# Kernel optimization log

Hardware: AMD Instinct MI355X
Metric: run time of the kernel (lower is better)

Reference implementation:

```python
import jax, jax.numpy as jnp
import numpy as np

N_EMBD = 768
HEAD_SIZE = 64

def setup_inputs() -> dict:
    key = jax.random.key(0)
    ks = jax.random.split(key, 9)
    B, S = 8, 2048
    scale = 1.0 / np.sqrt(N_EMBD)
    return {
        "q": jax.random.normal(ks[0], (B, S, N_EMBD), jnp.float32),
        "k": jax.random.normal(ks[1], (B, S, N_EMBD), jnp.float32),
        "v": jax.random.normal(ks[2], (B, S, N_EMBD), jnp.float32),
        "Wq": jax.random.normal(ks[3], (N_EMBD, HEAD_SIZE), jnp.float32) * scale,
        "bq": jnp.zeros((HEAD_SIZE,), jnp.float32),
        "Wk": jax.random.normal(ks[4], (N_EMBD, HEAD_SIZE), jnp.float32) * scale,
        "bk": jnp.zeros((HEAD_SIZE,), jnp.float32),
        "Wv": jax.random.normal(ks[5], (N_EMBD, HEAD_SIZE), jnp.float32) * scale,
        "bv": jnp.zeros((HEAD_SIZE,), jnp.float32),
    }

def reference(q, k, v, Wq, bq, Wk, bk, Wv, bv):
    # NOTE: original scales by sqrt(C) where C = n_embd (input dim), not head_size.
    C = q.shape[-1]
    qi = q @ Wq + bq  # [B,S,H]
    ki = k @ Wk + bk
    vi = v @ Wv + bv
    att = jnp.einsum('bsh,bth->bst', qi, ki) / jnp.sqrt(jnp.float32(C))
    att = jax.nn.softmax(att, axis=-1)
    out = jnp.einsum('bst,bth->bsh', att, vi)
    return out
```

## Files before the change

kernel.cpp:

```cpp
#include <hip/hip_runtime.h>

#define Bn 8
#define Sn 2048
#define Cn 768
#define Hn 64

typedef __attribute__((ext_vector_type(8))) short bf16x8;
typedef __attribute__((ext_vector_type(4))) float f32x4;

__device__ __forceinline__ unsigned short f2bf(float x) {
  unsigned int u = __builtin_bit_cast(unsigned int, x);
  u += 0x7FFFu + ((u >> 16) & 1u);
  return (unsigned short)(u >> 16);
}

__global__ __launch_bounds__(256) void wconv(const float* __restrict__ Wq,
                                             const float* __restrict__ Wk,
                                             const float* __restrict__ Wv,
                                             unsigned short* __restrict__ Wt) {
  int idx = blockIdx.x * 256 + threadIdx.x;
  int mat = idx / (Cn * Hn);
  int rem = idx - mat * (Cn * Hn);
  int c = rem / Hn, h = rem - c * Hn;
  const float* W = (mat == 0) ? Wq : (mat == 1) ? Wk : Wv;
  Wt[mat * (Hn * Cn) + h * Cn + c] = f2bf(W[rem]);
}

__global__ __launch_bounds__(256) void proj(const float* __restrict__ q,
                                            const float* __restrict__ k,
                                            const float* __restrict__ v,
                                            const float* __restrict__ bq,
                                            const float* __restrict__ bk,
                                            const float* __restrict__ bv,
                                            const unsigned short* __restrict__ Wt,
                                            unsigned short* __restrict__ qi,
                                            unsigned short* __restrict__ ki,
                                            unsigned short* __restrict__ vi) {
  const int mat  = blockIdx.x >> 8;
  const int row0 = (blockIdx.x & 255) * 64;
  const float* X    = (mat == 0) ? q  : (mat == 1) ? k  : v;
  const float* bias = (mat == 0) ? bq : (mat == 1) ? bk : bv;
  unsigned short* Y = (mat == 0) ? qi : (mat == 1) ? ki : vi;
  const unsigned short* Wm = Wt + mat * (Hn * Cn);
  const float scale = (mat == 0) ? 0.03608439182435161f : 1.0f;

  __shared__ __align__(16) unsigned char Xs[64 * 128];
  __shared__ __align__(16) unsigned char Ws[64 * 128];

  const int tid  = threadIdx.x;
  const int lane = tid & 63;
  const int w    = tid >> 6;
  const int col  = lane & 15;
  const int grp  = lane >> 4;

  f32x4 acc[4] = {};

  for (int kc = 0; kc < 12; ++kc) {
    __syncthreads();
#pragma unroll
    for (int i = 0; i < 4; ++i) {
      int f4 = tid + i * 256;
      int r  = f4 >> 4;
      int c4 = f4 & 15;
      float4 xv = *(const float4*)(X + (size_t)(row0 + r) * Cn + kc * 64 + c4 * 4);
      ushort4 hv;
      hv.x = f2bf(xv.x); hv.y = f2bf(xv.y); hv.z = f2bf(xv.z); hv.w = f2bf(xv.w);
      *(ushort4*)(Xs + r * 128 + ((c4 * 8) ^ ((r & 7) << 4))) = hv;
    }
    {
      int r = tid >> 2;
      int p = tid & 3;
      const uint4* src = (const uint4*)(Wm + (size_t)r * Cn + kc * 64);
      uint4 a  = src[p * 2];
      uint4 b2 = src[p * 2 + 1];
      *(uint4*)(Ws + r * 128 + ((p * 32) ^ ((r & 7) << 4)))        = a;
      *(uint4*)(Ws + r * 128 + (((p * 32) + 16) ^ ((r & 7) << 4))) = b2;
    }
    __syncthreads();
    const int rloc = w * 16 + col;
#pragma unroll
    for (int ks = 0; ks < 2; ++ks) {
      bf16x8 a = *(const bf16x8*)(Xs + rloc * 128 + ((ks * 64 + grp * 16) ^ ((rloc & 7) << 4)));
#pragma unroll
      for (int nf = 0; nf < 4; ++nf) {
        int wr = nf * 16 + col;
        bf16x8 bfr = *(const bf16x8*)(Ws + wr * 128 + ((ks * 64 + grp * 16) ^ ((wr & 7) << 4)));
        acc[nf] = __builtin_amdgcn_mfma_f32_16x16x32_bf16(a, bfr, acc[nf], 0, 0, 0);
      }
    }
  }
#pragma unroll
  for (int nf = 0; nf < 4; ++nf) {
    int h = nf * 16 + col;
    float bv = bias[h];
#pragma unroll
    for (int r2 = 0; r2 < 4; ++r2) {
      int row = row0 + w * 16 + grp * 4 + r2;
      Y[(size_t)row * Hn + h] = f2bf((acc[nf][r2] + bv) * scale);
    }
  }
}

__global__ __launch_bounds__(256) void attn(const unsigned short* __restrict__ qi,
                                            const unsigned short* __restrict__ ki,
                                            const unsigned short* __restrict__ vi,
                                            float* __restrict__ out) {
  const int b  = blockIdx.x >> 5;
  const int s0 = (blockIdx.x & 31) * 64;
  const unsigned short* Qb = qi + ((size_t)b * Sn + s0) * Hn;
  const unsigned short* Kb = ki + (size_t)b * Sn * Hn;
  const unsigned short* Vb = vi + (size_t)b * Sn * Hn;

  __shared__ __align__(16) unsigned char Ks[64 * 128];
  __shared__ __align__(16) unsigned char Vt[64 * 128];
  __shared__ __align__(16) unsigned char Ps[4 * 16 * 128];

  const int tid  = threadIdx.x;
  const int lane = tid & 63;
  const int w    = tid >> 6;
  const int col  = lane & 15;
  const int grp  = lane >> 4;

  bf16x8 qa[2];
#pragma unroll
  for (int ks2 = 0; ks2 < 2; ++ks2)
    qa[ks2] = *(const bf16x8*)(Qb + (size_t)(w * 16 + col) * Hn + ks2 * 32 + grp * 8);

  f32x4 acc[4] = {};
  float m[4], l[4];
#pragma unroll
  for (int r = 0; r < 4; ++r) { m[r] = -1e30f; l[r] = 0.0f; }

  for (int t = 0; t < Sn / 64; ++t) {
    const unsigned short* Kt = Kb + t * 64 * Hn;
    const unsigned short* Vg = Vb + t * 64 * Hn;
    __syncthreads();
    {
      int kr = tid >> 2, p = tid & 3;
      const uint4* src = (const uint4*)(Kt + kr * Hn);
      uint4 a  = src[p * 2];
      uint4 b2 = src[p * 2 + 1];
      *(uint4*)(Ks + kr * 128 + ((p * 32) ^ ((kr & 7) << 4)))        = a;
      *(uint4*)(Ks + kr * 128 + (((p * 32) + 16) ^ ((kr & 7) << 4))) = b2;
    }
    {
      int kp = tid >> 3;
      int dg = tid & 7;
      uint4 v0 = *(const uint4*)(Vg + (2 * kp) * Hn + dg * 8);
      uint4 v1 = *(const uint4*)(Vg + (2 * kp + 1) * Hn + dg * 8);
      const unsigned short* a0 = (const unsigned short*)&v0;
      const unsigned short* a1 = (const unsigned short*)&v1;
#pragma unroll
      for (int j0 = 0; j0 < 8; ++j0) {
        int j = (j0 + dg) & 7;
        int d = dg * 8 + j;
        unsigned int pk = (unsigned int)a0[j] | ((unsigned int)a1[j] << 16);
        *(unsigned int*)(Vt + d * 128 + ((4 * kp) ^ ((d & 7) << 4))) = pk;
      }
    }
    __syncthreads();
    f32x4 sf[4] = {};
#pragma unroll
    for (int ks2 = 0; ks2 < 2; ++ks2) {
#pragma unroll
      for (int nf = 0; nf < 4; ++nf) {
        int kr = nf * 16 + col;
        bf16x8 bfr = *(const bf16x8*)(Ks + kr * 128 + ((ks2 * 64 + grp * 16) ^ ((kr & 7) << 4)));
        sf[nf] = __builtin_amdgcn_mfma_f32_16x16x32_bf16(qa[ks2], bfr, sf[nf], 0, 0, 0);
      }
    }
    float mn[4], fs[4];
#pragma unroll
    for (int r = 0; r < 4; ++r) {
      float mx = fmaxf(fmaxf(sf[0][r], sf[1][r]), fmaxf(sf[2][r], sf[3][r]));
#pragma unroll
      for (int off = 1; off < 16; off <<= 1)
        mx = fmaxf(mx, __shfl_xor(mx, off, 64));
      mn[r] = fmaxf(m[r], mx);
      fs[r] = __expf(m[r] - mn[r]);
      m[r]  = mn[r];
    }
#pragma unroll
    for (int nf = 0; nf < 4; ++nf)
#pragma unroll
      for (int r = 0; r < 4; ++r)
        sf[nf][r] = __expf(sf[nf][r] - mn[r]);
#pragma unroll
    for (int r = 0; r < 4; ++r) {
      float sm = sf[0][r] + sf[1][r] + sf[2][r] + sf[3][r];
#pragma unroll
      for (int off = 1; off < 16; off <<= 1)
        sm += __shfl_xor(sm, off, 64);
      l[r] = l[r] * fs[r] + sm;
    }
#pragma unroll
    for (int nf = 0; nf < 4; ++nf) {
#pragma unroll
      for (int r = 0; r < 4; ++r) {
        acc[nf][r] *= fs[r];
        int prow = grp * 4 + r;
        int key  = nf * 16 + col;
        *(unsigned short*)(Ps + w * 2048 + prow * 128 + ((key * 2) ^ ((prow & 7) << 4))) =
            f2bf(sf[nf][r]);
      }
    }
    __syncthreads();
#pragma unroll
    for (int kk = 0; kk < 2; ++kk) {
      bf16x8 pa = *(const bf16x8*)(Ps + w * 2048 + col * 128 +
                                   ((kk * 64 + grp * 16) ^ ((col & 7) << 4)));
#pragma unroll
      for (int nf = 0; nf < 4; ++nf) {
        int dr = nf * 16 + col;
        bf16x8 bv = *(const bf16x8*)(Vt + dr * 128 + ((kk * 64 + grp * 16) ^ ((dr & 7) << 4)));
        acc[nf] = __builtin_amdgcn_mfma_f32_16x16x32_bf16(pa, bv, acc[nf], 0, 0, 0);
      }
    }
  }
#pragma unroll
  for (int nf = 0; nf < 4; ++nf) {
#pragma unroll
    for (int r = 0; r < 4; ++r) {
      int row = s0 + w * 16 + grp * 4 + r;
      out[((size_t)b * Sn + row) * Hn + nf * 16 + col] = acc[nf][r] / l[r];
    }
  }
}

extern "C" void kernel_launch(void* const* d_in, const int* in_sizes, int n_in,
                              void* d_out, int out_size, void* d_ws, size_t ws_size,
                              hipStream_t stream) {
  const float* q  = (const float*)d_in[0];
  const float* k  = (const float*)d_in[1];
  const float* v  = (const float*)d_in[2];
  const float* Wq = (const float*)d_in[3];
  const float* bq = (const float*)d_in[4];
  const float* Wk = (const float*)d_in[5];
  const float* bk = (const float*)d_in[6];
  const float* Wv = (const float*)d_in[7];
  const float* bv = (const float*)d_in[8];
  float* out = (float*)d_out;

  unsigned short* Wt = (unsigned short*)d_ws;
  unsigned short* qi = Wt + 3 * Hn * Cn;
  unsigned short* ki = qi + (size_t)Bn * Sn * Hn;
  unsigned short* vi = ki + (size_t)Bn * Sn * Hn;

  wconv<<<dim3((3 * Cn * Hn) / 256), dim3(256), 0, stream>>>(Wq, Wk, Wv, Wt);
  proj<<<dim3(768), dim3(256), 0, stream>>>(q, k, v, bq, bk, bv, Wt, qi, ki, vi);
  attn<<<dim3(Bn * (Sn / 64)), dim3(256), 0, stream>>>(qi, ki, vi, out);
}
```

Measured before the change: 108.5 us.

## Split attention over key tiles and merge partial softmax results in a combine kernel

The attention kernel now divides the key/value sequence into up to four splits. Each block writes unnormalised partial outputs along with its running max and sum to workspace, and a new combine kernel rescales and merges them. The aim is to raise the block count above one per CU so latency is better hidden. The cost is an extra launch and extra global traffic for the partial results. The change also removes a barrier before the P·V step, since the P tile in shared memory is private to each wave. If the workspace is too small, the code falls back to the unsplit kernel.

```diff
diff --git a/kernel.cpp b/kernel.cpp
--- a/kernel.cpp
+++ b/kernel.cpp
@@ -4,6 +4,7 @@
 #define Sn 2048
 #define Cn 768
 #define Hn 64
+#define BS (Bn * Sn)
 
 typedef __attribute__((ext_vector_type(8))) short bf16x8;
 typedef __attribute__((ext_vector_type(4))) float f32x4;
@@ -101,12 +102,20 @@
   }
 }
 
+template <int SPLIT>
 __global__ __launch_bounds__(256) void attn(const unsigned short* __restrict__ qi,
                                             const unsigned short* __restrict__ ki,
                                             const unsigned short* __restrict__ vi,
-                                            float* __restrict__ out) {
-  const int b  = blockIdx.x >> 5;
-  const int s0 = (blockIdx.x & 31) * 64;
+                                            float* __restrict__ pacc,
+                                            float* __restrict__ pm,
+                                            float* __restrict__ pl,
+                                            float* __restrict__ out,
+                                            int tpb) {
+  const int bq    = blockIdx.x & 255;
+  const int split = blockIdx.x >> 8;
+  const int b  = bq >> 5;
+  const int s0 = (bq & 31) * 64;
+  const int t0 = split * tpb;
   const unsigned short* Qb = qi + ((size_t)b * Sn + s0) * Hn;
   const unsigned short* Kb = ki + (size_t)b * Sn * Hn;
   const unsigned short* Vb = vi + (size_t)b * Sn * Hn;
@@ -131,7 +140,7 @@
 #pragma unroll
   for (int r = 0; r < 4; ++r) { m[r] = -1e30f; l[r] = 0.0f; }
 
-  for (int t = 0; t < Sn / 64; ++t) {
+  for (int t = t0; t < t0 + tpb; ++t) {
     const unsigned short* Kt = Kb + t * 64 * Hn;
     const unsigned short* Vg = Vb + t * 64 * Hn;
     __syncthreads();
@@ -204,7 +213,6 @@
             f2bf(sf[nf][r]);
       }
     }
-    __syncthreads();
 #pragma unroll
     for (int kk = 0; kk < 2; ++kk) {
       bf16x8 pa = *(const bf16x8*)(Ps + w * 2048 + col * 128 +
@@ -217,14 +225,57 @@
       }
     }
   }
-#pragma unroll
-  for (int nf = 0; nf < 4; ++nf) {
-#pragma unroll
-    for (int r = 0; r < 4; ++r) {
-      int row = s0 + w * 16 + grp * 4 + r;
-      out[((size_t)b * Sn + row) * Hn + nf * 16 + col] = acc[nf][r] / l[r];
-    }
-  }
+  if (SPLIT) {
+    const size_t sb = (size_t)split * BS + (size_t)b * Sn;
+#pragma unroll
+    for (int nf = 0; nf < 4; ++nf) {
+#pragma unroll
+      for (int r = 0; r < 4; ++r) {
+        int row = s0 + w * 16 + grp * 4 + r;
+        pacc[(sb + row) * Hn + nf * 16 + col] = acc[nf][r];
+      }
+    }
+    if (col == 0) {
+#pragma unroll
+      for (int r = 0; r < 4; ++r) {
+        int row = s0 + w * 16 + grp * 4 + r;
+        pm[sb + row] = m[r];
+        pl[sb + row] = l[r];
+      }
+    }
+  } else {
+#pragma unroll
+    for (int nf = 0; nf < 4; ++nf) {
+#pragma unroll
+      for (int r = 0; r < 4; ++r) {
+        int row = s0 + w * 16 + grp * 4 + r;
+        out[((size_t)b * Sn + row) * Hn + nf * 16 + col] = acc[nf][r] / l[r];
+      }
+    }
+  }
+}
+
+__global__ __launch_bounds__(256) void combine(const float* __restrict__ pacc,
+                                               const float* __restrict__ pm,
+                                               const float* __restrict__ pl,
+                                               float* __restrict__ out,
+                                               int nsplit) {
+  int gid = blockIdx.x * 256 + threadIdx.x;
+  int gr  = gid >> 4;
+  int dq  = (gid & 15) * 4;
+  float M = -1e30f;
+  for (int s = 0; s < nsplit; ++s) M = fmaxf(M, pm[(size_t)s * BS + gr]);
+  float L = 0.0f;
+  float4 o = make_float4(0.f, 0.f, 0.f, 0.f);
+  for (int s = 0; s < nsplit; ++s) {
+    float wgt = __expf(pm[(size_t)s * BS + gr] - M);
+    L += pl[(size_t)s * BS + gr] * wgt;
+    float4 p = *(const float4*)(pacc + ((size_t)s * BS + gr) * Hn + dq);
+    o.x += p.x * wgt; o.y += p.y * wgt; o.z += p.z * wgt; o.w += p.w * wgt;
+  }
+  float inv = 1.0f / L;
+  float4 r = make_float4(o.x * inv, o.y * inv, o.z * inv, o.w * inv);
+  *(float4*)(out + (size_t)gr * Hn + dq) = r;
 }
 
 extern "C" void kernel_launch(void* const* d_in, const int* in_sizes, int n_in,
@@ -243,10 +294,27 @@
 
   unsigned short* Wt = (unsigned short*)d_ws;
   unsigned short* qi = Wt + 3 * Hn * Cn;
-  unsigned short* ki = qi + (size_t)Bn * Sn * Hn;
-  unsigned short* vi = ki + (size_t)Bn * Sn * Hn;
+  unsigned short* ki = qi + (size_t)BS * Hn;
+  unsigned short* vi = ki + (size_t)BS * Hn;
+  float* pacc = (float*)(vi + (size_t)BS * Hn);
+
+  const size_t base_bytes = (size_t)(3 * Hn * Cn + 3 * (size_t)BS * Hn) * 2;
+  int nsplit = 4;
+  while (nsplit > 1 &&
+         base_bytes + (size_t)nsplit * ((size_t)BS * Hn * 4 + 2 * (size_t)BS * 4) > ws_size)
+    nsplit >>= 1;
+  bool direct = (base_bytes + (size_t)nsplit * ((size_t)BS * Hn * 4 + 2 * (size_t)BS * 4) > ws_size);
+
+  float* pm = pacc + (size_t)nsplit * BS * Hn;
+  float* pl = pm + (size_t)nsplit * BS;
 
   wconv<<<dim3((3 * Cn * Hn) / 256), dim3(256), 0, stream>>>(Wq, Wk, Wv, Wt);
   proj<<<dim3(768), dim3(256), 0, stream>>>(q, k, v, bq, bk, bv, Wt, qi, ki, vi);
-  attn<<<dim3(Bn * (Sn / 64)), dim3(256), 0, stream>>>(qi, ki, vi, out);
-}
+  if (direct) {
+    attn<0><<<dim3(256), dim3(256), 0, stream>>>(qi, ki, vi, nullptr, nullptr, nullptr, out, 32);
+  } else {
+    attn<1><<<dim3(256 * nsplit), dim3(256), 0, stream>>>(qi, ki, vi, pacc, pm, pl, nullptr,
+                                                          32 / nsplit);
+    combine<<<dim3(BS * 16 / 256), dim3(256), 0, stream>>>(pacc, pm, pl, out, nsplit);
+  }
+}
```

Result: faster. 87.75 us (-19.1%).
